# Performance work log

Hardware: AMD Instinct MI355X
Metric: run time of the kernel (lower is better)

The kernel has to match this reference:

```python
import jax, jax.numpy as jnp
import numpy as np

D_MODEL = 1024
NHEAD = 16
HEAD_DIM = D_MODEL // NHEAD
D_FF = 4096
BATCH = 2
SEQ = 2048
EPS = 1e-5


def _layer_norm(x, gamma, beta):
    mu = jnp.mean(x, axis=-1, keepdims=True)
    var = jnp.mean(jnp.square(x - mu), axis=-1, keepdims=True)
    return (x - mu) * jax.lax.rsqrt(var + EPS) * gamma + beta


def setup_inputs() -> dict:
    key = jax.random.key(0)
    ks = jax.random.split(key, 20)
    s = 0.02
    inp = {
        "src": jax.random.normal(ks[0], (BATCH, SEQ, D_MODEL), jnp.float32),
        "relative_bias": jax.random.normal(ks[1], (NHEAD, SEQ, SEQ), jnp.float32),
        "Wq": jax.random.normal(ks[2], (D_MODEL, D_MODEL), jnp.float32) * s,
        "bq": jnp.zeros((D_MODEL,), jnp.float32),
        "Wk": jax.random.normal(ks[3], (D_MODEL, D_MODEL), jnp.float32) * s,
        "bk": jnp.zeros((D_MODEL,), jnp.float32),
        "Wv": jax.random.normal(ks[4], (D_MODEL, D_MODEL), jnp.float32) * s,
        "bv": jnp.zeros((D_MODEL,), jnp.float32),
        "Wo": jax.random.normal(ks[5], (D_MODEL, D_MODEL), jnp.float32) * s,
        "bo": jnp.zeros((D_MODEL,), jnp.float32),
        "W1": jax.random.normal(ks[6], (D_FF, D_MODEL), jnp.float32) * s,
        "b1": jnp.zeros((D_FF,), jnp.float32),
        "W2": jax.random.normal(ks[7], (D_MODEL, D_FF), jnp.float32) * s,
        "b2": jnp.zeros((D_MODEL,), jnp.float32),
        "g1": jnp.ones((D_MODEL,), jnp.float32),
        "be1": jnp.zeros((D_MODEL,), jnp.float32),
        "g2": jnp.ones((D_MODEL,), jnp.float32),
        "be2": jnp.zeros((D_MODEL,), jnp.float32),
    }
    return inp


def reference(src, relative_bias, Wq, bq, Wk, bk, Wv, bv, Wo, bo,
              W1, b1, W2, b2, g1, be1, g2, be2):
    B, S, _ = src.shape
    # QKV projections -> [B, H, S, Dh]
    def proj(W, b):
        y = src @ W.T + b
        return y.reshape(B, S, NHEAD, HEAD_DIM).transpose(0, 2, 1, 3)
    q, k, v = proj(Wq, bq), proj(Wk, bk), proj(Wv, bv)
    scale = jnp.float32(np.sqrt(HEAD_DIM))
    # full score matrix + additive relative-position bias (PAPE)
    scores = jnp.einsum('bhqd,bhkd->bhqk', q, k) / scale + relative_bias[None]
    probs = jax.nn.softmax(scores, axis=-1)
    attn = jnp.einsum('bhqk,bhkd->bhqd', probs, v)
    attn = attn.transpose(0, 2, 1, 3).reshape(B, S, D_MODEL)
    attn = attn @ Wo.T + bo
    # residual + norm1
    x = _layer_norm(src + attn, g1, be1)
    # FFN (exact GELU, as torch nn.GELU default)
    h = jax.nn.gelu(x @ W1.T + b1, approximate=False)
    ff = h @ W2.T + b2
    # residual + norm2
    return _layer_norm(x + ff, g2, be2)
```

## Files before the change

kernel.cpp:

```cpp
#include <hip/hip_runtime.h>
#include <math.h>


using bf16_t = __bf16;
using bf16x8 = __attribute__((ext_vector_type(8))) __bf16;
using bf16x4 = __attribute__((ext_vector_type(4))) __bf16;
using f32x4  = __attribute__((ext_vector_type(4))) float;

#define DEV_INLINE __device__ __forceinline__

DEV_INLINE void lds_load16(const void* g, void* l) {
  __builtin_amdgcn_global_load_lds(
      (__attribute__((address_space(1))) void*)(g),
      (__attribute__((address_space(3))) void*)(l), 16, 0, 0);
}

DEV_INLINE bf16x8 lds_read8_sw(const bf16_t* base, int row, int chunk) {
  return *(const bf16x8*)((const char*)base + row * 128 + (((chunk) ^ (row & 7)) << 4));
}

__global__ __launch_bounds__(256)
void cast7_k(const float* __restrict__ s0, const float* __restrict__ s1,
             const float* __restrict__ s2, const float* __restrict__ s3,
             const float* __restrict__ s4, const float* __restrict__ s5,
             const float* __restrict__ s6,
             bf16_t* __restrict__ d0, bf16_t* __restrict__ d1,
             bf16_t* __restrict__ d2, bf16_t* __restrict__ d3,
             bf16_t* __restrict__ d4, bf16_t* __restrict__ d5,
             bf16_t* __restrict__ d6) {
  int i = (blockIdx.x * 256 + threadIdx.x) * 4;
  const float* s; bf16_t* d; int o;
  if (i < 4194304)       { s = s0; d = d0; o = i; }
  else if (i < 5242880)  { s = s1; d = d1; o = i - 4194304; }
  else if (i < 6291456)  { s = s2; d = d2; o = i - 5242880; }
  else if (i < 7340032)  { s = s3; d = d3; o = i - 6291456; }
  else if (i < 8388608)  { s = s4; d = d4; o = i - 7340032; }
  else if (i < 12582912) { s = s5; d = d5; o = i - 8388608; }
  else                   { s = s6; d = d6; o = i - 12582912; }
  float4 v = *(const float4*)(s + o);
  bf16x4 ob = {(bf16_t)v.x, (bf16_t)v.y, (bf16_t)v.z, (bf16_t)v.w};
  *(bf16x4*)(d + o) = ob;
}

__global__ __launch_bounds__(256)
void copy3_k(const float* __restrict__ a, const float* __restrict__ b,
             const float* __restrict__ c, float* __restrict__ d) {
  int i = blockIdx.x * 256 + threadIdx.x;
  const float* s = (i < 1024) ? a : ((i < 2048) ? b : c);
  int o = (i < 1024) ? i : ((i < 2048) ? i - 1024 : i - 2048);
  d[i] = s[o];
}

template <int MODE>
__global__ __launch_bounds__(256)
void gemm_bt(const bf16_t* __restrict__ A, int lda,
             const bf16_t* __restrict__ Bw, int ldb,
             const float* __restrict__ bias,
             void* __restrict__ outp, int M, int N, int K) {
  __shared__ bf16_t sA[2][128 * 32];
  __shared__ bf16_t sB[2][128 * 32];

  const int tid  = threadIdx.x;
  const int lane = tid & 63, wid = tid >> 6;
  const int wr = wid >> 1, wc = wid & 1;
  const int lm = lane & 15, lk = lane >> 4;
  const int z = blockIdx.z;

  int flat = blockIdx.y * gridDim.x + blockIdx.x;
  const int nwg = gridDim.x * gridDim.y;
  const int qq  = nwg >> 3;
  flat = (flat & 7) * qq + (flat >> 3);
  const int brow = flat / gridDim.x;
  const int bcol = flat % gridDim.x;

  A  += (size_t)z * K;
  Bw += (size_t)z * K;

  f32x4 zero = {0.f, 0.f, 0.f, 0.f};
  f32x4 acc[4][4];
#pragma unroll
  for (int i = 0; i < 4; ++i)
#pragma unroll
    for (int j = 0; j < 4; ++j) acc[i][j] = zero;

  const int srow = wid * 16 + (lane >> 2);
  const int scol = (lane & 3) * 8;
  const bf16_t* Abase = A  + (size_t)(brow * 128 + srow) * lda + scol;
  const bf16_t* Bbase = Bw + (size_t)(bcol * 128 + srow) * ldb + scol;

  auto stage = [&](int kk, int buf) {
    char* a = (char*)sA + buf * 8192 + wid * 1024;
    char* b = (char*)sB + buf * 8192 + wid * 1024;
    lds_load16(Abase + kk,                    a);
    lds_load16(Abase + (size_t)64 * lda + kk, a + 4096);
    lds_load16(Bbase + kk,                    b);
    lds_load16(Bbase + (size_t)64 * ldb + kk, b + 4096);
  };

  stage(0, 0);
  asm volatile("s_waitcnt vmcnt(0)" ::: "memory");
  __builtin_amdgcn_s_barrier();
  asm volatile("" ::: "memory");

  for (int kk = 0; kk < K; kk += 32) {
    const int cur = (kk >> 5) & 1;
    if (kk + 32 < K) stage(kk + 32, cur ^ 1);
    __builtin_amdgcn_sched_barrier(0);

    const bf16_t* Acur = &sA[cur][0];
    const bf16_t* Bcur = &sB[cur][0];
    bf16x8 a[4], b[4];
#pragma unroll
    for (int mi = 0; mi < 4; ++mi)
      a[mi] = *(const bf16x8*)(Acur + (wr * 64 + mi * 16 + lm) * 32 + lk * 8);
#pragma unroll
    for (int ni = 0; ni < 4; ++ni)
      b[ni] = *(const bf16x8*)(Bcur + (wc * 64 + ni * 16 + lm) * 32 + lk * 8);
    __builtin_amdgcn_s_setprio(1);
#pragma unroll
    for (int mi = 0; mi < 4; ++mi)
#pragma unroll
      for (int ni = 0; ni < 4; ++ni)
        acc[mi][ni] = __builtin_amdgcn_mfma_f32_16x16x32_bf16(a[mi], b[ni], acc[mi][ni], 0, 0, 0);
    __builtin_amdgcn_s_setprio(0);

    asm volatile("s_waitcnt vmcnt(0)" ::: "memory");
    __builtin_amdgcn_s_barrier();
    asm volatile("" ::: "memory");
  }

#pragma unroll
  for (int mi = 0; mi < 4; ++mi) {
#pragma unroll
    for (int ni = 0; ni < 4; ++ni) {
#pragma unroll
      for (int j = 0; j < 4; ++j) {
        int row = brow * 128 + wr * 64 + mi * 16 + lk * 4 + j;
        int col = bcol * 128 + wc * 64 + ni * 16 + lm;
        if (MODE == 3) {
          ((float*)outp)[(size_t)z * M * N + (size_t)row * N + col] = acc[mi][ni][j];
        } else {
          float v = acc[mi][ni][j] + bias[col];
          if (MODE == 1) v = 0.5f * v * (1.f + erff(v * 0.70710678118f));
          ((bf16_t*)outp)[(size_t)row * N + col] = (bf16_t)v;
        }
      }
    }
  }
}

__global__ __launch_bounds__(256)
void transpose_v(const bf16_t* __restrict__ qkv, bf16_t* __restrict__ vt) {
  __shared__ bf16_t tile[64][65];
  const int bid = blockIdx.x;
  const int st = bid & 31, h = (bid >> 5) & 15, b = bid >> 9;
  const int tid = threadIdx.x;
  const int r = tid >> 3, c0 = (tid & 7) * 8;
#pragma unroll
  for (int p = 0; p < 2; ++p) {
    int rr = p * 32 + r;
    const bf16_t* g = qkv + (size_t)(b * 2048 + st * 64 + rr) * 3072 + 2048 + h * 64 + c0;
    bf16x8 v = *(const bf16x8*)g;
#pragma unroll
    for (int i = 0; i < 8; ++i) tile[rr][c0 + i] = v[i];
  }
  __syncthreads();
#pragma unroll
  for (int p = 0; p < 2; ++p) {
    int d = p * 32 + r;
    bf16x8 o;
#pragma unroll
    for (int i = 0; i < 8; ++i) o[i] = tile[c0 + i][d];
    *(bf16x8*)(vt + ((size_t)(b * 16 + h) * 64 + d) * 2048 + st * 64 + c0) = o;
  }
}

__global__ __launch_bounds__(512, 2)
void attn_k(const bf16_t* __restrict__ qkv, const bf16_t* __restrict__ vt,
            const float* __restrict__ bias, bf16_t* __restrict__ outp) {
  __shared__ bf16_t Ks[2][64 * 64];
  __shared__ bf16_t Vs[2][64 * 64];
  __shared__ bf16_t Ps[8][16 * 64];
  __shared__ float  Bs[8][16 * 64];

  const int bid = blockIdx.x;
  const int x  = bid & 7;
  const int r_ = bid >> 3;
  const int h  = x * 2 + (r_ & 1);
  const int b  = (r_ >> 1) & 1;
  const int qt = r_ >> 2;

  const int tid = threadIdx.x;
  const int lane = tid & 63, wid = tid >> 6;
  const int lm = lane & 15, lk = lane >> 4;

  const int sr  = tid >> 3;
  const int sc_ = (((tid & 7) ^ (sr & 7)) * 8);
  const bf16_t* kgb = qkv + 1024 + (size_t)(b * 2048 + sr) * 3072 + h * 64 + sc_;
  const bf16_t* vgb = vt + ((size_t)((b * 16 + h) * 64) + sr) * 2048 + sc_;

  auto stageKV = [&](int kt, int buf) {
    lds_load16(kgb + (size_t)(kt * 64) * 3072, (char*)Ks + buf * 8192 + wid * 1024);
    lds_load16(vgb + kt * 64,                  (char*)Vs + buf * 8192 + wid * 1024);
  };

  const char* brow_base = (const char*)(bias +
      ((size_t)h * 2048 + qt * 128 + wid * 16 + (lane >> 4)) * 2048);
  const char* bsrc0 = brow_base + ((lane & 15) << 4);
  const char* bsrc1 = brow_base + (((lane & 15) ^ 4) << 4);
  char* BsWb = (char*)Bs + wid * 4096;

  auto biasStage = [&](int kt) {
    const size_t co = (size_t)kt * 256;
    lds_load16(bsrc0 + co,          BsWb);
    lds_load16(bsrc1 + co + 32768,  BsWb + 1024);
    lds_load16(bsrc0 + co + 65536,  BsWb + 2048);
    lds_load16(bsrc1 + co + 98304,  BsWb + 3072);
  };

  bf16x8 qa[2];
#pragma unroll
  for (int ks = 0; ks < 2; ++ks)
    qa[ks] = *(const bf16x8*)(qkv +
        (size_t)(b * 2048 + qt * 128 + wid * 16 + lm) * 3072 + h * 64 + ks * 32 + lk * 8);

  f32x4 zero = {0.f, 0.f, 0.f, 0.f};
  f32x4 acc_o[4];
  float l_run[4];
#pragma unroll
  for (int j = 0; j < 4; ++j) { acc_o[j] = zero; l_run[j] = 0.f; }

  bf16_t* PsW = &Ps[wid][0];
  const float* BsW = &Bs[wid][0];

  stageKV(0, 0);
  biasStage(0);
  asm volatile("s_waitcnt vmcnt(0)" ::: "memory");
  __builtin_amdgcn_s_barrier();
  asm volatile("" ::: "memory");

  for (int kt = 0; kt < 32; ++kt) {
    const int cur = kt & 1;
    const int ktn = (kt + 1 < 32) ? kt + 1 : 31;
    stageKV(ktn, cur ^ 1);
    __builtin_amdgcn_sched_barrier(0);

    const bf16_t* Kcur = (const bf16_t*)((const char*)Ks + cur * 8192);
    const bf16_t* Vcur = (const bf16_t*)((const char*)Vs + cur * 8192);

    f32x4 sc[4];
#pragma unroll
    for (int ni = 0; ni < 4; ++ni) sc[ni] = zero;
    __builtin_amdgcn_s_setprio(1);
#pragma unroll
    for (int ks = 0; ks < 2; ++ks) {
#pragma unroll
      for (int ni = 0; ni < 4; ++ni) {
        bf16x8 kb = lds_read8_sw(Kcur, ni * 16 + lm, ks * 4 + lk);
        sc[ni] = __builtin_amdgcn_mfma_f32_16x16x32_bf16(qa[ks], kb, sc[ni], 0, 0, 0);
      }
    }
    __builtin_amdgcn_s_setprio(0);

    asm volatile("s_waitcnt vmcnt(2)" ::: "memory");

    float rs[4];
#pragma unroll
    for (int j = 0; j < 4; ++j) rs[j] = 0.f;
#pragma unroll
    for (int ni = 0; ni < 4; ++ni)
#pragma unroll
      for (int j = 0; j < 4; ++j) {
        float s = sc[ni][j] * 0.125f +
            *(const float*)((const char*)BsW + (lk * 4 + j) * 256 +
                            (((ni * 4 + (lm >> 2)) ^ ((lk & 1) << 2)) << 4) + (lm & 3) * 4);
        sc[ni][j] = __expf(s);
        rs[j] += sc[ni][j];
      }
#pragma unroll
    for (int off = 1; off < 16; off <<= 1)
#pragma unroll
      for (int j = 0; j < 4; ++j)
        rs[j] += __shfl_xor(rs[j], off, 64);
#pragma unroll
    for (int j = 0; j < 4; ++j) l_run[j] += rs[j];

    __builtin_amdgcn_sched_barrier(0);
    biasStage(ktn);
    __builtin_amdgcn_sched_barrier(0);

#pragma unroll
    for (int ni = 0; ni < 4; ++ni)
#pragma unroll
      for (int j = 0; j < 4; ++j) {
        int rr = lk * 4 + j;
        *(bf16_t*)((char*)PsW + rr * 128 + (((ni * 2 + (lm >> 3)) ^ (rr & 7)) << 4) + (lm & 7) * 2)
            = (bf16_t)sc[ni][j];
      }

#pragma unroll
    for (int ks = 0; ks < 2; ++ks) {
      bf16x8 pa = lds_read8_sw(PsW, lm, ks * 4 + lk);
      __builtin_amdgcn_s_setprio(1);
#pragma unroll
      for (int nf = 0; nf < 4; ++nf) {
        bf16x8 vb = lds_read8_sw(Vcur, nf * 16 + lm, ks * 4 + lk);
        acc_o[nf] = __builtin_amdgcn_mfma_f32_16x16x32_bf16(pa, vb, acc_o[nf], 0, 0, 0);
      }
      __builtin_amdgcn_s_setprio(0);
    }

    asm volatile("s_waitcnt vmcnt(4)" ::: "memory");
    __builtin_amdgcn_s_barrier();
    asm volatile("" ::: "memory");
  }

#pragma unroll
  for (int nf = 0; nf < 4; ++nf) {
#pragma unroll
    for (int j = 0; j < 4; ++j) {
      float o = acc_o[nf][j] / l_run[j];
      outp[(size_t)(b * 2048 + qt * 128 + wid * 16 + lk * 4 + j) * 1024 + h * 64 + nf * 16 + lm] = (bf16_t)o;
    }
  }
}

__global__ __launch_bounds__(256)
void layernorm2_k(const float* __restrict__ pa, const float* __restrict__ pb,
                  const float* __restrict__ bias, const float* __restrict__ resid,
                  const float* __restrict__ gamma, const float* __restrict__ beta,
                  float* __restrict__ out32, bf16_t* __restrict__ out16) {
  const int row = blockIdx.x, tid = threadIdx.x;
  const int lane = tid & 63, wid = tid >> 6;
  const size_t base = (size_t)row * 1024;
  float4 v  = ((const float4*)(pa + base))[tid];
  float4 v2 = ((const float4*)(pb + base))[tid];
  float4 bb = ((const float4*)bias)[tid];
  float4 rr = ((const float4*)(resid + base))[tid];
  v.x += v2.x + bb.x + rr.x;
  v.y += v2.y + bb.y + rr.y;
  v.z += v2.z + bb.z + rr.z;
  v.w += v2.w + bb.w + rr.w;
  float s  = v.x + v.y + v.z + v.w;
  float s2 = v.x * v.x + v.y * v.y + v.z * v.z + v.w * v.w;
#pragma unroll
  for (int off = 32; off; off >>= 1) {
    s  += __shfl_xor(s, off, 64);
    s2 += __shfl_xor(s2, off, 64);
  }
  __shared__ float red[8];
  if (lane == 0) { red[wid] = s; red[wid + 4] = s2; }
  __syncthreads();
  s  = red[0] + red[1] + red[2] + red[3];
  s2 = red[4] + red[5] + red[6] + red[7];
  const float mu  = s * (1.f / 1024.f);
  const float inv = rsqrtf(s2 * (1.f / 1024.f) - mu * mu + 1e-5f);
  const float4 g4 = ((const float4*)gamma)[tid];
  const float4 b4 = ((const float4*)beta)[tid];
  float4 o;
  o.x = (v.x - mu) * inv * g4.x + b4.x;
  o.y = (v.y - mu) * inv * g4.y + b4.y;
  o.z = (v.z - mu) * inv * g4.z + b4.z;
  o.w = (v.w - mu) * inv * g4.w + b4.w;
  ((float4*)(out32 + base))[tid] = o;
  if (out16) {
    bf16x4 ob = {(bf16_t)o.x, (bf16_t)o.y, (bf16_t)o.z, (bf16_t)o.w};
    *(bf16x4*)(out16 + base + tid * 4) = ob;
  }
}

extern "C" void kernel_launch(void* const* d_in, const int* in_sizes, int n_in,
                              void* d_out, int out_size, void* d_ws, size_t ws_size,
                              hipStream_t stream) {
  const float* src  = (const float*)d_in[0];
  const float* rbias= (const float*)d_in[1];
  const float* Wq   = (const float*)d_in[2];
  const float* bq   = (const float*)d_in[3];
  const float* Wk   = (const float*)d_in[4];
  const float* bk   = (const float*)d_in[5];
  const float* Wv   = (const float*)d_in[6];
  const float* bv   = (const float*)d_in[7];
  const float* Wo   = (const float*)d_in[8];
  const float* bo   = (const float*)d_in[9];
  const float* W1   = (const float*)d_in[10];
  const float* b1   = (const float*)d_in[11];
  const float* W2   = (const float*)d_in[12];
  const float* b2   = (const float*)d_in[13];
  const float* g1   = (const float*)d_in[14];
  const float* be1  = (const float*)d_in[15];
  const float* g2   = (const float*)d_in[16];
  const float* be2  = (const float*)d_in[17];

  char* ws = (char*)d_ws;
  const size_t MB = 1u << 20;
  bf16_t* src_bf  = (bf16_t*)(ws + 0);
  bf16_t* wqkv_bf = (bf16_t*)(ws + 8 * MB);
  bf16_t* wo_bf   = (bf16_t*)(ws + 14 * MB);
  bf16_t* w1_bf   = (bf16_t*)(ws + 16 * MB);
  bf16_t* w2_bf   = (bf16_t*)(ws + 24 * MB);
  float*  bqkv    = (float*)(ws + 32 * MB);
  bf16_t* qkv_bf  = (bf16_t*)(ws + 33 * MB);
  bf16_t* vt      = (bf16_t*)(ws + 57 * MB);
  bf16_t* attn_bf = (bf16_t*)(ws + 65 * MB);
  float*  pA      = (float*)(ws + 73 * MB);
  float*  pB      = (float*)(ws + 89 * MB);
  float*  xf      = (float*)(ws + 105 * MB);
  bf16_t* x_bf    = (bf16_t*)(ws + 121 * MB);
  bf16_t* h_bf    = (bf16_t*)(ws + 129 * MB);

  cast7_k<<<16384, 256, 0, stream>>>(
      src, Wq, Wk, Wv, Wo, W1, W2,
      src_bf, wqkv_bf, wqkv_bf + 1024 * 1024, wqkv_bf + 2 * 1024 * 1024,
      wo_bf, w1_bf, w2_bf);
  copy3_k<<<12, 256, 0, stream>>>(bq, bk, bv, bqkv);

  gemm_bt<0><<<dim3(24, 32), 256, 0, stream>>>(
      src_bf, 1024, wqkv_bf, 1024, bqkv, qkv_bf, 4096, 3072, 1024);
  transpose_v<<<1024, 256, 0, stream>>>(qkv_bf, vt);
  attn_k<<<512, 512, 0, stream>>>(qkv_bf, vt, rbias, attn_bf);

  gemm_bt<3><<<dim3(8, 32, 2), 256, 0, stream>>>(
      attn_bf, 1024, wo_bf, 1024, nullptr, pA, 4096, 1024, 512);
  layernorm2_k<<<4096, 256, 0, stream>>>(pA, pB, bo, src, g1, be1, xf, x_bf);

  gemm_bt<1><<<dim3(32, 32), 256, 0, stream>>>(
      x_bf, 1024, w1_bf, 1024, b1, h_bf, 4096, 4096, 1024);

  gemm_bt<3><<<dim3(8, 32, 2), 256, 0, stream>>>(
      h_bf, 4096, w2_bf, 4096, nullptr, pA, 4096, 1024, 2048);
  layernorm2_k<<<4096, 256, 0, stream>>>(pA, pB, b2, xf, g2, be2, (float*)d_out, nullptr);
}
```

Measured before the change: 335.0 us.

## Fuse V transpose into QKV GEMM epilogue and bias copy into cast kernel

The QKV GEMM epilogue now writes the V columns straight into the transposed per-head layout, which removes the separate transpose_v kernel and its extra read and write of V. The bias concatenation is folded into the cast kernel, dropping one more launch. In the attention loop the exp and row-sum are moved after the bias-staging call, so the next bias tile's loads can overlap with the exp work. The transposed epilogue stores are strided per element (a stride of 2048 along the sequence), so they may coalesce poorly and slow the GEMM epilogue.

```diff
diff --git a/kernel.cpp b/kernel.cpp
--- a/kernel.cpp
+++ b/kernel.cpp
@@ -20,15 +20,25 @@
 }
 
 __global__ __launch_bounds__(256)
-void cast7_k(const float* __restrict__ s0, const float* __restrict__ s1,
+void cast8_k(const float* __restrict__ s0, const float* __restrict__ s1,
              const float* __restrict__ s2, const float* __restrict__ s3,
              const float* __restrict__ s4, const float* __restrict__ s5,
              const float* __restrict__ s6,
+             const float* __restrict__ b0, const float* __restrict__ b1,
+             const float* __restrict__ b2,
              bf16_t* __restrict__ d0, bf16_t* __restrict__ d1,
              bf16_t* __restrict__ d2, bf16_t* __restrict__ d3,
              bf16_t* __restrict__ d4, bf16_t* __restrict__ d5,
-             bf16_t* __restrict__ d6) {
+             bf16_t* __restrict__ d6, float* __restrict__ db) {
   int i = (blockIdx.x * 256 + threadIdx.x) * 4;
+  if (i >= 16777216) {
+    int o = i - 16777216;
+    if (o >= 3072) return;
+    const float* s = (o < 1024) ? b0 : ((o < 2048) ? b1 : b2);
+    int oo = (o < 1024) ? o : ((o < 2048) ? o - 1024 : o - 2048);
+    *(float4*)(db + o) = *(const float4*)(s + oo);
+    return;
+  }
   const float* s; bf16_t* d; int o;
   if (i < 4194304)       { s = s0; d = d0; o = i; }
   else if (i < 5242880)  { s = s1; d = d1; o = i - 4194304; }
@@ -42,21 +52,13 @@
   *(bf16x4*)(d + o) = ob;
 }
 
-__global__ __launch_bounds__(256)
-void copy3_k(const float* __restrict__ a, const float* __restrict__ b,
-             const float* __restrict__ c, float* __restrict__ d) {
-  int i = blockIdx.x * 256 + threadIdx.x;
-  const float* s = (i < 1024) ? a : ((i < 2048) ? b : c);
-  int o = (i < 1024) ? i : ((i < 2048) ? i - 1024 : i - 2048);
-  d[i] = s[o];
-}
-
 template <int MODE>
 __global__ __launch_bounds__(256)
 void gemm_bt(const bf16_t* __restrict__ A, int lda,
              const bf16_t* __restrict__ Bw, int ldb,
              const float* __restrict__ bias,
-             void* __restrict__ outp, int M, int N, int K) {
+             void* __restrict__ outp, bf16_t* __restrict__ vt,
+             int M, int N, int K) {
   __shared__ bf16_t sA[2][128 * 32];
   __shared__ bf16_t sB[2][128 * 32];
 
@@ -129,6 +131,7 @@
     asm volatile("" ::: "memory");
   }
 
+  const bool vmode = (MODE == 0) && (vt != nullptr) && (bcol >= 16);
 #pragma unroll
   for (int mi = 0; mi < 4; ++mi) {
 #pragma unroll
@@ -142,36 +145,16 @@
         } else {
           float v = acc[mi][ni][j] + bias[col];
           if (MODE == 1) v = 0.5f * v * (1.f + erff(v * 0.70710678118f));
-          ((bf16_t*)outp)[(size_t)row * N + col] = (bf16_t)v;
+          if (vmode) {
+            int c2 = col - 2048;
+            int bb = row >> 11, s = row & 2047;
+            vt[((size_t)(bb * 16 + (c2 >> 6)) * 64 + (c2 & 63)) * 2048 + s] = (bf16_t)v;
+          } else {
+            ((bf16_t*)outp)[(size_t)row * N + col] = (bf16_t)v;
+          }
         }
       }
     }
-  }
-}
-
-__global__ __launch_bounds__(256)
-void transpose_v(const bf16_t* __restrict__ qkv, bf16_t* __restrict__ vt) {
-  __shared__ bf16_t tile[64][65];
-  const int bid = blockIdx.x;
-  const int st = bid & 31, h = (bid >> 5) & 15, b = bid >> 9;
-  const int tid = threadIdx.x;
-  const int r = tid >> 3, c0 = (tid & 7) * 8;
-#pragma unroll
-  for (int p = 0; p < 2; ++p) {
-    int rr = p * 32 + r;
-    const bf16_t* g = qkv + (size_t)(b * 2048 + st * 64 + rr) * 3072 + 2048 + h * 64 + c0;
-    bf16x8 v = *(const bf16x8*)g;
-#pragma unroll
-    for (int i = 0; i < 8; ++i) tile[rr][c0 + i] = v[i];
-  }
-  __syncthreads();
-#pragma unroll
-  for (int p = 0; p < 2; ++p) {
-    int d = p * 32 + r;
-    bf16x8 o;
-#pragma unroll
-    for (int i = 0; i < 8; ++i) o[i] = tile[c0 + i][d];
-    *(bf16x8*)(vt + ((size_t)(b * 16 + h) * 64 + d) * 2048 + st * 64 + c0) = o;
   }
 }
 
@@ -264,30 +247,35 @@
 
     asm volatile("s_waitcnt vmcnt(2)" ::: "memory");
 
-    float rs[4];
-#pragma unroll
-    for (int j = 0; j < 4; ++j) rs[j] = 0.f;
 #pragma unroll
     for (int ni = 0; ni < 4; ++ni)
 #pragma unroll
-      for (int j = 0; j < 4; ++j) {
-        float s = sc[ni][j] * 0.125f +
+      for (int j = 0; j < 4; ++j)
+        sc[ni][j] = sc[ni][j] * 0.125f +
             *(const float*)((const char*)BsW + (lk * 4 + j) * 256 +
                             (((ni * 4 + (lm >> 2)) ^ ((lk & 1) << 2)) << 4) + (lm & 3) * 4);
-        sc[ni][j] = __expf(s);
-        rs[j] += sc[ni][j];
-      }
-#pragma unroll
-    for (int off = 1; off < 16; off <<= 1)
-#pragma unroll
-      for (int j = 0; j < 4; ++j)
-        rs[j] += __shfl_xor(rs[j], off, 64);
-#pragma unroll
-    for (int j = 0; j < 4; ++j) l_run[j] += rs[j];
 
     __builtin_amdgcn_sched_barrier(0);
     biasStage(ktn);
     __builtin_amdgcn_sched_barrier(0);
+
+    float rs[4];
+#pragma unroll
+    for (int j = 0; j < 4; ++j) rs[j] = 0.f;
+#pragma unroll
+    for (int ni = 0; ni < 4; ++ni)
+#pragma unroll
+      for (int j = 0; j < 4; ++j) {
+        sc[ni][j] = __expf(sc[ni][j]);
+        rs[j] += sc[ni][j];
+      }
+#pragma unroll
+    for (int off = 1; off < 16; off <<= 1)
+#pragma unroll
+      for (int j = 0; j < 4; ++j)
+        rs[j] += __shfl_xor(rs[j], off, 64);
+#pragma unroll
+    for (int j = 0; j < 4; ++j) l_run[j] += rs[j];
 
 #pragma unroll
     for (int ni = 0; ni < 4; ++ni)
@@ -408,25 +396,23 @@
   bf16_t* x_bf    = (bf16_t*)(ws + 121 * MB);
   bf16_t* h_bf    = (bf16_t*)(ws + 129 * MB);
 
-  cast7_k<<<16384, 256, 0, stream>>>(
-      src, Wq, Wk, Wv, Wo, W1, W2,
+  cast8_k<<<16387, 256, 0, stream>>>(
+      src, Wq, Wk, Wv, Wo, W1, W2, bq, bk, bv,
       src_bf, wqkv_bf, wqkv_bf + 1024 * 1024, wqkv_bf + 2 * 1024 * 1024,
-      wo_bf, w1_bf, w2_bf);
-  copy3_k<<<12, 256, 0, stream>>>(bq, bk, bv, bqkv);
+      wo_bf, w1_bf, w2_bf, bqkv);
 
   gemm_bt<0><<<dim3(24, 32), 256, 0, stream>>>(
-      src_bf, 1024, wqkv_bf, 1024, bqkv, qkv_bf, 4096, 3072, 1024);
-  transpose_v<<<1024, 256, 0, stream>>>(qkv_bf, vt);
+      src_bf, 1024, wqkv_bf, 1024, bqkv, qkv_bf, vt, 4096, 3072, 1024);
   attn_k<<<512, 512, 0, stream>>>(qkv_bf, vt, rbias, attn_bf);
 
   gemm_bt<3><<<dim3(8, 32, 2), 256, 0, stream>>>(
-      attn_bf, 1024, wo_bf, 1024, nullptr, pA, 4096, 1024, 512);
+      attn_bf, 1024, wo_bf, 1024, nullptr, pA, nullptr, 4096, 1024, 512);
   layernorm2_k<<<4096, 256, 0, stream>>>(pA, pB, bo, src, g1, be1, xf, x_bf);
 
   gemm_bt<1><<<dim3(32, 32), 256, 0, stream>>>(
-      x_bf, 1024, w1_bf, 1024, b1, h_bf, 4096, 4096, 1024);
+      x_bf, 1024, w1_bf, 1024, b1, h_bf, nullptr, 4096, 4096, 1024);
 
   gemm_bt<3><<<dim3(8, 32, 2), 256, 0, stream>>>(
-      h_bf, 4096, w2_bf, 4096, nullptr, pA, 4096, 1024, 2048);
+      h_bf, 4096, w2_bf, 4096, nullptr, pA, nullptr, 4096, 1024, 2048);
   layernorm2_k<<<4096, 256, 0, stream>>>(pA, pB, b2, xf, g2, be2, (float*)d_out, nullptr);
 }
```

Measured after the change: 333.0 us. About the same (-0.6%).
